# Kernel tuning notes

Hardware: AMD Instinct MI355X
Metric: run time of the kernel (lower is better)

## Reference

```python
import jax, jax.numpy as jnp
import numpy as np

ALPHA = 0.2  # leaky relu slope
NEG = -9e15  # mask fill value from the torch code


def gat_layer(x, adj_mask, W, a):
    """One dense GAT attention head.
    Equivalent math to the torch layer, without materializing the
    [N, N, 2F] a_input tensor: a^T [h_i ; h_j] = (h @ a1)_i + (h @ a2)_j.
    x: [N, Fin], adj_mask: [N, N] bool, W: [Fin, Fout], a: [2*Fout, 1].
    """
    h = x @ W                              # [N, Fout]
    Fo = W.shape[1]
    s_src = h @ a[:Fo, 0]                  # [N]
    s_dst = h @ a[Fo:, 0]                  # [N]
    e = jax.nn.leaky_relu(s_src[:, None] + s_dst[None, :], ALPHA)  # [N, N]
    e = jnp.where(adj_mask, e, NEG)
    attn = jax.nn.softmax(e, axis=1)       # dropout is a no-op in eval mode
    return attn @ h                        # [N, Fout]


def setup_inputs() -> dict:
    key = jax.random.key(0)
    ks = jax.random.split(key, 6)
    N, nfeat, nhid, nclass, nheads = 4096, 512, 64, 32, 8
    x = jax.random.normal(ks[0], (N, nfeat), dtype=jnp.float32)
    adj = jax.random.randint(ks[1], (N, N), 0, 2, dtype=jnp.int32)
    # params scaled like torch uniform(-1/sqrt(fan_in), 1/sqrt(fan_in))
    W_att = jax.random.normal(ks[2], (nheads, nfeat, nhid), dtype=jnp.float32) / np.sqrt(nfeat)
    a_att = jax.random.normal(ks[3], (nheads, 2 * nhid, 1), dtype=jnp.float32) / np.sqrt(2 * nhid)
    W_out = jax.random.normal(ks[4], (nhid * nheads, nclass), dtype=jnp.float32) / np.sqrt(nhid * nheads)
    a_out = jax.random.normal(ks[5], (2 * nclass, 1), dtype=jnp.float32) / np.sqrt(2 * nclass)
    return {"x": x, "adj": adj, "W_att": W_att, "a_att": a_att,
            "W_out": W_out, "a_out": a_out}


def reference(x, adj, W_att, a_att, W_out, a_out):
    adj_mask = adj > 0  # [N, N]
    # multi-head layer, concat=True => elu per head, concat along features
    heads = jax.vmap(lambda W, a: jax.nn.elu(gat_layer(x, adj_mask, W, a)))(W_att, a_att)  # [H, N, nhid]
    H, N, Fh = heads.shape
    hcat = jnp.transpose(heads, (1, 0, 2)).reshape(N, H * Fh)  # [N, H*nhid]
    # output layer, concat=False, then elu applied by GAT.forward
    out = jax.nn.elu(gat_layer(hcat, adj_mask, W_out, a_out))  # [N, nclass]
    return out
```

## Files before the change

### kernel.cpp

```cpp
#include <hip/hip_runtime.h>
#include <math.h>

#define NN 4096
#define CC 512
#define MB (1024*1024)
#define LOG2E 1.4426950408889634f

typedef __attribute__((ext_vector_type(8))) __bf16 bf16x8;
typedef __attribute__((ext_vector_type(4))) float f32x4;
typedef unsigned short ushort_t;
typedef unsigned int uint_t;
typedef unsigned char uchar_t;

#if __has_builtin(__builtin_amdgcn_exp2f)
#define EXP2(x) __builtin_amdgcn_exp2f(x)
#else
#define EXP2(x) exp2f(x)
#endif

static __device__ __forceinline__ float elu1(float x){ return x > 0.f ? x : (__expf(x)-1.f); }
static __device__ __forceinline__ ushort_t f2bf(float f){
    union { float f; uint_t u; } v; v.f = f;
    uint_t r = (v.u + 0x7FFFu + ((v.u >> 16) & 1u)) >> 16;
    return (ushort_t)r;
}
static __device__ __forceinline__ float bf2f(ushort_t h){
    union { uint_t u; float f; } q; q.u = ((uint_t)h) << 16; return q.f;
}

__global__ void k_prepW(const float* __restrict__ Watt,
                        ushort_t* __restrict__ Wh, ushort_t* __restrict__ Wl){
    int idx = blockIdx.x*256 + threadIdx.x;
    int c = idx >> 7, kq = idx & 127, k = kq*4;
    ushort4 h4, l4;
    float v[4];
    #pragma unroll
    for(int j=0;j<4;j++)
        v[j] = Watt[(c>>6)*(512*64) + (k+j)*64 + (c&63)];
    h4.x = f2bf(v[0]); h4.y = f2bf(v[1]); h4.z = f2bf(v[2]); h4.w = f2bf(v[3]);
    l4.x = f2bf(v[0]-bf2f(h4.x)); l4.y = f2bf(v[1]-bf2f(h4.y));
    l4.z = f2bf(v[2]-bf2f(h4.z)); l4.w = f2bf(v[3]-bf2f(h4.w));
    *(ushort4*)&Wh[(size_t)c*512 + k] = h4;
    *(ushort4*)&Wl[(size_t)c*512 + k] = l4;
}

__global__ void k_splitx(const float* __restrict__ x,
                         ushort_t* __restrict__ xh, ushort_t* __restrict__ xl){
    int idx = blockIdx.x*256 + threadIdx.x;
    float4 v = *(const float4*)&x[(size_t)idx*4];
    ushort4 h4, l4;
    h4.x = f2bf(v.x); h4.y = f2bf(v.y); h4.z = f2bf(v.z); h4.w = f2bf(v.w);
    l4.x = f2bf(v.x-bf2f(h4.x)); l4.y = f2bf(v.y-bf2f(h4.y));
    l4.z = f2bf(v.z-bf2f(h4.z)); l4.w = f2bf(v.w-bf2f(h4.w));
    *(ushort4*)&xh[(size_t)idx*4] = h4;
    *(ushort4*)&xl[(size_t)idx*4] = l4;
}

__global__ void k_pack(const int* __restrict__ adj, uint_t* __restrict__ abits){
    int idx = blockIdx.x*256 + threadIdx.x;
    int i = idx >> 7, q = idx & 127;
    const int4* p = (const int4*)&adj[(size_t)i*NN + q*32];
    uint_t m = 0;
    #pragma unroll
    for(int g=0; g<8; g++){
        int4 v = p[g];
        m |= (uint_t)(v.x > 0) << (g*4 + 0);
        m |= (uint_t)(v.y > 0) << (g*4 + 1);
        m |= (uint_t)(v.z > 0) << (g*4 + 2);
        m |= (uint_t)(v.w > 0) << (g*4 + 3);
    }
    abits[idx] = m;
}

__global__ __launch_bounds__(256) void k_gemm1(
        const ushort_t* __restrict__ xh, const ushort_t* __restrict__ xl,
        const ushort_t* __restrict__ Wh, const ushort_t* __restrict__ Wl,
        float* __restrict__ h_all, ushort_t* __restrict__ hT){
    const int t = threadIdx.x;
    const int l = t & 63, wv = t >> 6;
    const int lr = l & 15, lg = l >> 4;
    const int ib = blockIdx.x*64 + wv*16;
    const int j0 = blockIdx.y*64;

    f32x4 acc[4] = {};
    #pragma unroll 2
    for(int ks=0; ks<16; ks++){
        const int kb = ks*32 + lg*8;
        bf16x8 ah = *(const bf16x8*)&xh[(size_t)(ib+lr)*512 + kb];
        bf16x8 al = *(const bf16x8*)&xl[(size_t)(ib+lr)*512 + kb];
        bf16x8 bh[4], bl[4];
        #pragma unroll
        for(int nt=0;nt<4;nt++){
            bh[nt] = *(const bf16x8*)&Wh[(size_t)(j0+nt*16+lr)*512 + kb];
            bl[nt] = *(const bf16x8*)&Wl[(size_t)(j0+nt*16+lr)*512 + kb];
        }
        #pragma unroll
        for(int nt=0;nt<4;nt++){
            acc[nt] = __builtin_amdgcn_mfma_f32_16x16x32_bf16(ah, bh[nt], acc[nt], 0,0,0);
            acc[nt] = __builtin_amdgcn_mfma_f32_16x16x32_bf16(al, bh[nt], acc[nt], 0,0,0);
            acc[nt] = __builtin_amdgcn_mfma_f32_16x16x32_bf16(ah, bl[nt], acc[nt], 0,0,0);
        }
    }
    #pragma unroll
    for(int nt=0;nt<4;nt++){
        const int col = j0 + nt*16 + lr;
        #pragma unroll
        for(int r=0;r<4;r++)
            h_all[(size_t)(ib + lg*4 + r)*512 + col] = acc[nt][r];
        ushort4 o;
        o.x = f2bf(acc[nt][0]); o.y = f2bf(acc[nt][1]);
        o.z = f2bf(acc[nt][2]); o.w = f2bf(acc[nt][3]);
        *(ushort4*)&hT[(size_t)col*NN + ib + lg*4] = o;
    }
}

__global__ void k_scores1(const float* __restrict__ hall, const float* __restrict__ aatt,
                          float* __restrict__ ssrc2, float* __restrict__ sdst2){
    int t = threadIdx.x;
    int hd = t & 7, il = t >> 3;
    int i = blockIdx.x*32 + il;
    const float4* h4 = (const float4*)&hall[(size_t)i*CC + hd*64];
    const float4* a1 = (const float4*)&aatt[hd*128];
    const float4* a2 = (const float4*)&aatt[hd*128 + 64];
    float ss = 0.f, sd = 0.f;
    #pragma unroll
    for(int q=0;q<16;q++){
        float4 h = h4[q], u = a1[q], v = a2[q];
        ss += h.x*u.x + h.y*u.y + h.z*u.z + h.w*u.w;
        sd += h.x*v.x + h.y*v.y + h.z*v.z + h.w*v.w;
    }
    ssrc2[hd*NN + i] = ss*LOG2E;
    sdst2[hd*NN + i] = sd*LOG2E;
}

__global__ __launch_bounds__(256) void k_attn1(
        const ushort_t* __restrict__ hT,
        const float* __restrict__ ssrc2, const float* __restrict__ sdst2,
        const uchar_t* __restrict__ abits,
        float* __restrict__ pnumT, float* __restrict__ pden){
    const int t = threadIdx.x;
    const int l = t & 63, wv = t >> 6;
    const int hd0 = blockIdx.z*2;
    const int i0 = blockIdx.x*32;
    const int jcc = blockIdx.y;
    const int lr = l & 15, lg = l >> 4;

    f32x4 acc[2][2][4] = {};
    f32x4 dacc[2][2] = {};

    float ss[2][2];
    #pragma unroll
    for(int hd=0;hd<2;hd++)
        #pragma unroll
        for(int mh=0;mh<2;mh++)
            ss[hd][mh] = ssrc2[(hd0+hd)*NN + i0 + mh*16 + lr];

    bf16x8 ones;
    #pragma unroll
    for(int e=0;e<8;e++) ones[e] = (__bf16)1.0f;

    const int jwb = jcc*2048 + wv*512;
    const uchar_t* arow0 = &abits[(size_t)(i0 + lr)*512 + jcc*256 + wv*64];
    const uchar_t* arow1 = &abits[(size_t)(i0 + 16 + lr)*512 + jcc*256 + wv*64];

    bf16x8 bA[2][4], bB[2][4];
    float4 sdaA[2], sdbA[2], sdaB[2], sdbB[2];
    uint_t bitsA0, bitsA1, bitsB0, bitsB1;

#define LOAD1(SFX, JT) { \
    const int jb_ = jwb + (JT)*32 + lg*8; \
    _Pragma("unroll") \
    for(int hd=0;hd<2;hd++){ \
        _Pragma("unroll") \
        for(int nt=0;nt<4;nt++) \
            b##SFX[hd][nt] = *(const bf16x8*)&hT[(size_t)((hd0+hd)*64 + nt*16 + lr)*NN + jb_]; \
        sda##SFX[hd] = *(const float4*)&sdst2[(hd0+hd)*NN + jb_]; \
        sdb##SFX[hd] = *(const float4*)&sdst2[(hd0+hd)*NN + jb_ + 4]; \
    } \
    bits##SFX##0 = arow0[(JT)*4 + lg]; \
    bits##SFX##1 = arow1[(JT)*4 + lg]; }

#define COMP1(SFX) { \
    _Pragma("unroll") \
    for(int hd=0;hd<2;hd++){ \
        float sdv[8] = {sda##SFX[hd].x, sda##SFX[hd].y, sda##SFX[hd].z, sda##SFX[hd].w, \
                        sdb##SFX[hd].x, sdb##SFX[hd].y, sdb##SFX[hd].z, sdb##SFX[hd].w}; \
        _Pragma("unroll") \
        for(int mh=0;mh<2;mh++){ \
            const uint_t bits = mh ? bits##SFX##1 : bits##SFX##0; \
            bf16x8 a; \
            _Pragma("unroll") \
            for(int e=0;e<8;e++){ \
                float s_ = ss[hd][mh] + sdv[e]; \
                float t_ = fmaxf(s_, 0.2f*s_); \
                float w_ = EXP2(t_) * (float)((bits >> e) & 1u); \
                a[e] = (__bf16)w_; \
            } \
            _Pragma("unroll") \
            for(int nt=0;nt<4;nt++) \
                acc[hd][mh][nt] = __builtin_amdgcn_mfma_f32_16x16x32_bf16( \
                    a, b##SFX[hd][nt], acc[hd][mh][nt], 0, 0, 0); \
            dacc[hd][mh] = __builtin_amdgcn_mfma_f32_16x16x32_bf16( \
                    a, ones, dacc[hd][mh], 0, 0, 0); \
        } \
    } }

    LOAD1(A, 0);
    for(int jt=0; jt<16; jt+=2){
        LOAD1(B, jt+1);
        COMP1(A);
        if (jt + 2 < 16) LOAD1(A, jt+2);
        COMP1(B);
    }
#undef LOAD1
#undef COMP1

    __shared__ f32x4 red[2][20][64];
    __syncthreads();
    if (wv >= 2){
        #pragma unroll
        for(int hd=0;hd<2;hd++)
            #pragma unroll
            for(int mh=0;mh<2;mh++){
                #pragma unroll
                for(int nt=0;nt<4;nt++) red[wv-2][(hd*2+mh)*4+nt][l] = acc[hd][mh][nt];
                red[wv-2][16 + hd*2+mh][l] = dacc[hd][mh];
            }
    }
    __syncthreads();
    if (wv < 2){
        #pragma unroll
        for(int hd=0;hd<2;hd++)
            #pragma unroll
            for(int mh=0;mh<2;mh++){
                #pragma unroll
                for(int nt=0;nt<4;nt++) acc[hd][mh][nt] += red[wv][(hd*2+mh)*4+nt][l];
                dacc[hd][mh] += red[wv][16 + hd*2+mh][l];
            }
    }
    __syncthreads();
    if (wv == 1){
        #pragma unroll
        for(int hd=0;hd<2;hd++)
            #pragma unroll
            for(int mh=0;mh<2;mh++){
                #pragma unroll
                for(int nt=0;nt<4;nt++) red[0][(hd*2+mh)*4+nt][l] = acc[hd][mh][nt];
                red[0][16 + hd*2+mh][l] = dacc[hd][mh];
            }
    }
    __syncthreads();
    if (wv == 0){
        #pragma unroll
        for(int hd=0;hd<2;hd++)
            #pragma unroll
            for(int mh=0;mh<2;mh++){
                #pragma unroll
                for(int nt=0;nt<4;nt++){
                    f32x4 v = acc[hd][mh][nt] + red[0][(hd*2+mh)*4+nt][l];
                    int col = (hd0+hd)*64 + nt*16 + lr;
                    float4 o = {v[0], v[1], v[2], v[3]};
                    *(float4*)&pnumT[((size_t)jcc*512 + col)*NN + i0 + mh*16 + lg*4] = o;
                }
                f32x4 d = dacc[hd][mh] + red[0][16 + hd*2+mh][l];
                if (lr == 0){
                    #pragma unroll
                    for(int r=0;r<4;r++)
                        pden[((size_t)jcc*8 + hd0+hd)*NN + i0 + mh*16 + lg*4 + r] = d[r];
                }
            }
    }
}

__global__ void k_reduce1T(const float* __restrict__ pnumT, const float* __restrict__ pden,
                           float* __restrict__ hcatT){
    int idx = blockIdx.x*256 + threadIdx.x;
    int c = idx >> 12, i = idx & 4095, hd = c >> 6;
    float s = 0.f, d = 0.f;
    #pragma unroll
    for(int jc=0;jc<2;jc++){
        s += pnumT[((size_t)jc*512 + c)*NN + i];
        d += pden[((size_t)jc*8 + hd)*NN + i];
    }
    hcatT[(size_t)c*NN + i] = elu1(s/d);
}

__global__ __launch_bounds__(256) void k_gemm2(const float* __restrict__ AT,
                                               const float* __restrict__ B,
                                               const float* __restrict__ aout,
                                               ushort_t* __restrict__ h2T,
                                               float* __restrict__ ss2,
                                               float* __restrict__ sd2){
    __shared__ float As[32][32];
    __shared__ float Bs[32][32];
    const int t = threadIdx.x;
    const int i0 = blockIdx.x*32;
    const int ty = t >> 4, tx = t & 15;
    float acc[2][2] = {{0.f,0.f},{0.f,0.f}};
    for(int k0=0;k0<512;k0+=32){
        __syncthreads();
        { int k = t >> 3, i4 = (t & 7)*4;
          *(float4*)&As[k][i4] = *(const float4*)&AT[(size_t)(k0+k)*NN + i0 + i4]; }
        { int k = t >> 3, n4 = (t & 7)*4;
          *(float4*)&Bs[k][n4] = *(const float4*)&B[(size_t)(k0+k)*32 + n4]; }
        __syncthreads();
        #pragma unroll
        for(int k=0;k<32;k++){
            float2 a2 = *(const float2*)&As[k][ty*2];
            float2 b2 = *(const float2*)&Bs[k][tx*2];
            acc[0][0] += a2.x*b2.x; acc[0][1] += a2.x*b2.y;
            acc[1][0] += a2.y*b2.x; acc[1][1] += a2.y*b2.y;
        }
    }
    #pragma unroll
    for(int a=0;a<2;a++){
        #pragma unroll
        for(int b=0;b<2;b++)
            h2T[(size_t)(tx*2+b)*NN + i0 + ty*2 + a] = f2bf(acc[a][b]);
    }
    float a1x = aout[tx*2], a1y = aout[tx*2+1];
    float a2x = aout[32+tx*2], a2y = aout[32+tx*2+1];
    #pragma unroll
    for(int a=0;a<2;a++){
        float ps = acc[a][0]*a1x + acc[a][1]*a1y;
        float pd = acc[a][0]*a2x + acc[a][1]*a2y;
        #pragma unroll
        for(int m=1;m<16;m<<=1){
            ps += __shfl_xor(ps, m);
            pd += __shfl_xor(pd, m);
        }
        if (tx == 0){
            ss2[i0 + ty*2 + a] = ps*LOG2E;
            sd2[i0 + ty*2 + a] = pd*LOG2E;
        }
    }
}

__global__ __launch_bounds__(256) void k_attn2(
        const ushort_t* __restrict__ h2T,
        const float* __restrict__ ss2, const float* __restrict__ sd2,
        const uchar_t* __restrict__ abits,
        float* __restrict__ pnum2T, float* __restrict__ pden2){
    const int t = threadIdx.x;
    const int l = t & 63;
    const int wv = t >> 6;
    const int i0 = blockIdx.x*16;
    const int jc = blockIdx.y;
    const int lr = l & 15, lg = l >> 4;
    const int jcw = jc*4 + wv;

    f32x4 acc[2] = {};
    f32x4 dacc = {};
    const float ss = ss2[i0 + lr];
    bf16x8 ones;
    #pragma unroll
    for(int e=0;e<8;e++) ones[e] = (__bf16)1.0f;

    const uchar_t* arow = &abits[(size_t)(i0+lr)*512 + jc*128 + wv*4];

    bf16x8 bA[2], bB[2];
    float4 sdaA, sdbA, sdaB, sdbB;
    uint_t bitsA, bitsB;

#define LOAD2(SFX, JT) { \
    const int jb_ = jc*1024 + (JT)*128 + wv*32 + lg*8; \
    _Pragma("unroll") \
    for(int nt=0;nt<2;nt++) \
        b##SFX[nt] = *(const bf16x8*)&h2T[(size_t)(nt*16 + lr)*NN + jb_]; \
    sda##SFX = *(const float4*)&sd2[jb_]; \
    sdb##SFX = *(const float4*)&sd2[jb_ + 4]; \
    bits##SFX = arow[(JT)*16 + lg]; }

#define COMP2(SFX) { \
    float sdv[8] = {sda##SFX.x, sda##SFX.y, sda##SFX.z, sda##SFX.w, \
                    sdb##SFX.x, sdb##SFX.y, sdb##SFX.z, sdb##SFX.w}; \
    bf16x8 a; \
    _Pragma("unroll") \
    for(int e=0;e<8;e++){ \
        float s_ = ss + sdv[e]; \
        float t_ = fmaxf(s_, 0.2f*s_); \
        float w_ = EXP2(t_) * (float)((bits##SFX >> e) & 1u); \
        a[e] = (__bf16)w_; \
    } \
    _Pragma("unroll") \
    for(int nt=0;nt<2;nt++) \
        acc[nt] = __builtin_amdgcn_mfma_f32_16x16x32_bf16(a, b##SFX[nt], acc[nt], 0, 0, 0); \
    dacc = __builtin_amdgcn_mfma_f32_16x16x32_bf16(a, ones, dacc, 0, 0, 0); }

    LOAD2(A, 0);
    for(int jt=0; jt<8; jt+=2){
        LOAD2(B, jt+1);
        COMP2(A);
        if (jt + 2 < 8) LOAD2(A, jt+2);
        COMP2(B);
    }
#undef LOAD2
#undef COMP2

    #pragma unroll
    for(int nt=0;nt<2;nt++){
        int col = nt*16 + lr;
        float4 v = {acc[nt][0], acc[nt][1], acc[nt][2], acc[nt][3]};
        *(float4*)&pnum2T[((size_t)jcw*32 + col)*NN + i0 + lg*4] = v;
    }
    if (lr == 0){
        #pragma unroll
        for(int r=0;r<4;r++)
            pden2[(size_t)jcw*NN + i0 + lg*4 + r] = dacc[r];
    }
}

__global__ void k_reduce2(const float* __restrict__ pnum2T, const float* __restrict__ pden2,
                          float* __restrict__ out){
    int idx = blockIdx.x*256 + threadIdx.x;
    int c = idx >> 12, i = idx & 4095;
    float s = 0.f, d = 0.f;
    #pragma unroll
    for(int jcw=0;jcw<16;jcw++){
        s += pnum2T[((size_t)jcw*32 + c)*NN + i];
        d += pden2[(size_t)jcw*NN + i];
    }
    out[(size_t)i*32 + c] = elu1(s/d);
}

extern "C" void kernel_launch(void* const* d_in, const int* in_sizes, int n_in,
                              void* d_out, int out_size, void* d_ws, size_t ws_size,
                              hipStream_t stream){
    const float* x    = (const float*)d_in[0];
    const int*   adj  = (const int*)  d_in[1];
    const float* Watt = (const float*)d_in[2];
    const float* aatt = (const float*)d_in[3];
    const float* Wout = (const float*)d_in[4];
    const float* aout = (const float*)d_in[5];
    float* out = (float*)d_out;
    char* ws = (char*)d_ws;

    float*    h_all = (float*)   (ws + (size_t) 0*MB);
    float*    hcatT = (float*)   (ws + (size_t) 0*MB);
    ushort_t* Whi   = (ushort_t*)(ws + (size_t) 8*MB);
    ushort_t* Wlo   = (ushort_t*)(ws + (size_t) 8*MB + 512*1024);
    float*    ssrc2 = (float*)   (ws + (size_t) 9*MB);
    float*    sdst2 = (float*)   (ws + (size_t)10*MB);
    ushort_t* hT    = (ushort_t*)(ws + (size_t)11*MB);
    uint_t*   abits = (uint_t*)  (ws + (size_t)15*MB);
    float*    ss2   = (float*)   (ws + (size_t)18*MB);
    float*    sd2   = (float*)   (ws + (size_t)19*MB);
    ushort_t* h2T   = (ushort_t*)(ws + (size_t)20*MB);
    float*    pden  = (float*)   (ws + (size_t)21*MB);
    float*    pden2 = (float*)   (ws + (size_t)21*MB + 512*1024);
    float*    pnumT = (float*)   (ws + (size_t)22*MB);
    float*    pnum2T= pnumT;
    ushort_t* xh    = (ushort_t*)(ws + (size_t)38*MB);
    ushort_t* xl    = (ushort_t*)(ws + (size_t)42*MB);
    if (ws_size < (size_t)55*MB) return;

    k_prepW   <<<256, 256, 0, stream>>>(Watt, Whi, Wlo);
    k_splitx  <<<2048, 256, 0, stream>>>(x, xh, xl);
    k_pack    <<<2048, 256, 0, stream>>>(adj, abits);
    k_gemm1   <<<dim3(64,8), 256, 0, stream>>>(xh, xl, Whi, Wlo, h_all, hT);
    k_scores1 <<<128, 256, 0, stream>>>(h_all, aatt, ssrc2, sdst2);
    k_attn1   <<<dim3(128,2,4), 256, 0, stream>>>(hT, ssrc2, sdst2, (const uchar_t*)abits, pnumT, pden);
    k_reduce1T<<<8192, 256, 0, stream>>>(pnumT, pden, hcatT);
    k_gemm2   <<<128, 256, 0, stream>>>(hcatT, Wout, aout, h2T, ss2, sd2);
    k_attn2   <<<dim3(256,4), 256, 0, stream>>>(h2T, ss2, sd2, (const uchar_t*)abits, pnum2T, pden2);
    k_reduce2 <<<512, 256, 0, stream>>>(pnum2T, pden2, out);
}
```

Baseline: 299.4 us.

## Fuse score computation into GEMM1 and retile both attention kernels

Computes the source/destination attention scores in the GEMM1 epilogue with a lane-shuffle reduction, which removes the fp32 h_all write and the separate k_scores1 kernel. k_attn1 now processes one head per block with 64 rows instead of two heads with 32 rows. The j-dimension split changes from 2 to 4 chunks, so each loaded hT tile is reused across more rows. k_attn2 is retiled the same way, with 64 rows per block and a shared-memory cross-wave reduction, which halves the partial sums that k_reduce2 has to read. The cost is more accumulator registers per thread, which may lower occupancy, and more partial-sum traffic in the first reduce.

Result: faster. 263.0 us (-12.2%).

```diff
diff --git a/kernel.cpp b/kernel.cpp
--- a/kernel.cpp
+++ b/kernel.cpp
@@ -75,12 +75,15 @@
 __global__ __launch_bounds__(256) void k_gemm1(
         const ushort_t* __restrict__ xh, const ushort_t* __restrict__ xl,
         const ushort_t* __restrict__ Wh, const ushort_t* __restrict__ Wl,
-        float* __restrict__ h_all, ushort_t* __restrict__ hT){
+        const float* __restrict__ aatt,
+        ushort_t* __restrict__ hT,
+        float* __restrict__ ssrc2, float* __restrict__ sdst2){
     const int t = threadIdx.x;
     const int l = t & 63, wv = t >> 6;
     const int lr = l & 15, lg = l >> 4;
     const int ib = blockIdx.x*64 + wv*16;
-    const int j0 = blockIdx.y*64;
+    const int hd = blockIdx.y;
+    const int j0 = hd*64;
 
     f32x4 acc[4] = {};
     #pragma unroll 2
@@ -104,33 +107,31 @@
     #pragma unroll
     for(int nt=0;nt<4;nt++){
         const int col = j0 + nt*16 + lr;
-        #pragma unroll
-        for(int r=0;r<4;r++)
-            h_all[(size_t)(ib + lg*4 + r)*512 + col] = acc[nt][r];
         ushort4 o;
         o.x = f2bf(acc[nt][0]); o.y = f2bf(acc[nt][1]);
         o.z = f2bf(acc[nt][2]); o.w = f2bf(acc[nt][3]);
         *(ushort4*)&hT[(size_t)col*NN + ib + lg*4] = o;
     }
-}
-
-__global__ void k_scores1(const float* __restrict__ hall, const float* __restrict__ aatt,
-                          float* __restrict__ ssrc2, float* __restrict__ sdst2){
-    int t = threadIdx.x;
-    int hd = t & 7, il = t >> 3;
-    int i = blockIdx.x*32 + il;
-    const float4* h4 = (const float4*)&hall[(size_t)i*CC + hd*64];
-    const float4* a1 = (const float4*)&aatt[hd*128];
-    const float4* a2 = (const float4*)&aatt[hd*128 + 64];
-    float ss = 0.f, sd = 0.f;
-    #pragma unroll
-    for(int q=0;q<16;q++){
-        float4 h = h4[q], u = a1[q], v = a2[q];
-        ss += h.x*u.x + h.y*u.y + h.z*u.z + h.w*u.w;
-        sd += h.x*v.x + h.y*v.y + h.z*v.z + h.w*v.w;
-    }
-    ssrc2[hd*NN + i] = ss*LOG2E;
-    sdst2[hd*NN + i] = sd*LOG2E;
+    float a1v[4], a2v[4];
+    #pragma unroll
+    for(int nt=0;nt<4;nt++){
+        a1v[nt] = aatt[hd*128 + nt*16 + lr];
+        a2v[nt] = aatt[hd*128 + 64 + nt*16 + lr];
+    }
+    #pragma unroll
+    for(int r=0;r<4;r++){
+        float ps = acc[0][r]*a1v[0] + acc[1][r]*a1v[1] + acc[2][r]*a1v[2] + acc[3][r]*a1v[3];
+        float pd = acc[0][r]*a2v[0] + acc[1][r]*a2v[1] + acc[2][r]*a2v[2] + acc[3][r]*a2v[3];
+        #pragma unroll
+        for(int m=1;m<16;m<<=1){
+            ps += __shfl_xor(ps, m);
+            pd += __shfl_xor(pd, m);
+        }
+        if (lr == 0){
+            ssrc2[hd*NN + ib + lg*4 + r] = ps*LOG2E;
+            sdst2[hd*NN + ib + lg*4 + r] = pd*LOG2E;
+        }
+    }
 }
 
 __global__ __launch_bounds__(256) void k_attn1(
@@ -140,76 +141,71 @@
         float* __restrict__ pnumT, float* __restrict__ pden){
     const int t = threadIdx.x;
     const int l = t & 63, wv = t >> 6;
-    const int hd0 = blockIdx.z*2;
-    const int i0 = blockIdx.x*32;
+    const int hd = blockIdx.z;
+    const int i0 = blockIdx.x*64;
     const int jcc = blockIdx.y;
     const int lr = l & 15, lg = l >> 4;
 
-    f32x4 acc[2][2][4] = {};
-    f32x4 dacc[2][2] = {};
-
-    float ss[2][2];
-    #pragma unroll
-    for(int hd=0;hd<2;hd++)
-        #pragma unroll
-        for(int mh=0;mh<2;mh++)
-            ss[hd][mh] = ssrc2[(hd0+hd)*NN + i0 + mh*16 + lr];
+    f32x4 acc[4][4] = {};
+    f32x4 dacc[4] = {};
+
+    float ss[4];
+    #pragma unroll
+    for(int mh=0;mh<4;mh++)
+        ss[mh] = ssrc2[hd*NN + i0 + mh*16 + lr];
 
     bf16x8 ones;
     #pragma unroll
     for(int e=0;e<8;e++) ones[e] = (__bf16)1.0f;
 
-    const int jwb = jcc*2048 + wv*512;
-    const uchar_t* arow0 = &abits[(size_t)(i0 + lr)*512 + jcc*256 + wv*64];
-    const uchar_t* arow1 = &abits[(size_t)(i0 + 16 + lr)*512 + jcc*256 + wv*64];
-
-    bf16x8 bA[2][4], bB[2][4];
-    float4 sdaA[2], sdbA[2], sdaB[2], sdbB[2];
-    uint_t bitsA0, bitsA1, bitsB0, bitsB1;
+    const int jwb = jcc*1024 + wv*256;
+    const uchar_t* arow[4];
+    #pragma unroll
+    for(int mh=0;mh<4;mh++)
+        arow[mh] = &abits[(size_t)(i0 + mh*16 + lr)*512 + (jwb >> 3)];
+
+    bf16x8 bA[4], bB[4];
+    float4 sdaA, sdbA, sdaB, sdbB;
+    uint_t bitsA[4], bitsB[4];
 
 #define LOAD1(SFX, JT) { \
     const int jb_ = jwb + (JT)*32 + lg*8; \
     _Pragma("unroll") \
-    for(int hd=0;hd<2;hd++){ \
+    for(int nt=0;nt<4;nt++) \
+        b##SFX[nt] = *(const bf16x8*)&hT[(size_t)(hd*64 + nt*16 + lr)*NN + jb_]; \
+    sda##SFX = *(const float4*)&sdst2[hd*NN + jb_]; \
+    sdb##SFX = *(const float4*)&sdst2[hd*NN + jb_ + 4]; \
+    _Pragma("unroll") \
+    for(int mh=0;mh<4;mh++) \
+        bits##SFX[mh] = arow[mh][(JT)*4 + lg]; }
+
+#define COMP1(SFX) { \
+    float sdv[8] = {sda##SFX.x, sda##SFX.y, sda##SFX.z, sda##SFX.w, \
+                    sdb##SFX.x, sdb##SFX.y, sdb##SFX.z, sdb##SFX.w}; \
+    _Pragma("unroll") \
+    for(int mh=0;mh<4;mh++){ \
+        const uint_t bits = bits##SFX[mh]; \
+        bf16x8 a; \
+        _Pragma("unroll") \
+        for(int e=0;e<8;e++){ \
+            float s_ = ss[mh] + sdv[e]; \
+            float t_ = fmaxf(s_, 0.2f*s_); \
+            float w_ = EXP2(t_) * (float)((bits >> e) & 1u); \
+            a[e] = (__bf16)w_; \
+        } \
         _Pragma("unroll") \
         for(int nt=0;nt<4;nt++) \
-            b##SFX[hd][nt] = *(const bf16x8*)&hT[(size_t)((hd0+hd)*64 + nt*16 + lr)*NN + jb_]; \
-        sda##SFX[hd] = *(const float4*)&sdst2[(hd0+hd)*NN + jb_]; \
-        sdb##SFX[hd] = *(const float4*)&sdst2[(hd0+hd)*NN + jb_ + 4]; \
-    } \
-    bits##SFX##0 = arow0[(JT)*4 + lg]; \
-    bits##SFX##1 = arow1[(JT)*4 + lg]; }
-
-#define COMP1(SFX) { \
-    _Pragma("unroll") \
-    for(int hd=0;hd<2;hd++){ \
-        float sdv[8] = {sda##SFX[hd].x, sda##SFX[hd].y, sda##SFX[hd].z, sda##SFX[hd].w, \
-                        sdb##SFX[hd].x, sdb##SFX[hd].y, sdb##SFX[hd].z, sdb##SFX[hd].w}; \
-        _Pragma("unroll") \
-        for(int mh=0;mh<2;mh++){ \
-            const uint_t bits = mh ? bits##SFX##1 : bits##SFX##0; \
-            bf16x8 a; \
-            _Pragma("unroll") \
-            for(int e=0;e<8;e++){ \
-                float s_ = ss[hd][mh] + sdv[e]; \
-                float t_ = fmaxf(s_, 0.2f*s_); \
-                float w_ = EXP2(t_) * (float)((bits >> e) & 1u); \
-                a[e] = (__bf16)w_; \
-            } \
-            _Pragma("unroll") \
-            for(int nt=0;nt<4;nt++) \
-                acc[hd][mh][nt] = __builtin_amdgcn_mfma_f32_16x16x32_bf16( \
-                    a, b##SFX[hd][nt], acc[hd][mh][nt], 0, 0, 0); \
-            dacc[hd][mh] = __builtin_amdgcn_mfma_f32_16x16x32_bf16( \
-                    a, ones, dacc[hd][mh], 0, 0, 0); \
-        } \
+            acc[mh][nt] = __builtin_amdgcn_mfma_f32_16x16x32_bf16( \
+                a, b##SFX[nt], acc[mh][nt], 0, 0, 0); \
+        dacc[mh] = __builtin_amdgcn_mfma_f32_16x16x32_bf16( \
+                a, ones, dacc[mh], 0, 0, 0); \
     } }
 
     LOAD1(A, 0);
-    for(int jt=0; jt<16; jt+=2){
+    for(int jt=0; jt<8; jt+=2){
         LOAD1(B, jt+1);
         COMP1(A);
-        if (jt + 2 < 16) LOAD1(A, jt+2);
+        if (jt + 2 < 8) LOAD1(A, jt+2);
         COMP1(B);
     }
 #undef LOAD1
@@ -219,56 +215,48 @@
     __syncthreads();
     if (wv >= 2){
         #pragma unroll
-        for(int hd=0;hd<2;hd++)
-            #pragma unroll
-            for(int mh=0;mh<2;mh++){
+        for(int mh=0;mh<4;mh++){
+            #pragma unroll
+            for(int nt=0;nt<4;nt++) red[wv-2][mh*4+nt][l] = acc[mh][nt];
+            red[wv-2][16+mh][l] = dacc[mh];
+        }
+    }
+    __syncthreads();
+    if (wv < 2){
+        #pragma unroll
+        for(int mh=0;mh<4;mh++){
+            #pragma unroll
+            for(int nt=0;nt<4;nt++) acc[mh][nt] += red[wv][mh*4+nt][l];
+            dacc[mh] += red[wv][16+mh][l];
+        }
+    }
+    __syncthreads();
+    if (wv == 1){
+        #pragma unroll
+        for(int mh=0;mh<4;mh++){
+            #pragma unroll
+            for(int nt=0;nt<4;nt++) red[0][mh*4+nt][l] = acc[mh][nt];
+            red[0][16+mh][l] = dacc[mh];
+        }
+    }
+    __syncthreads();
+    if (wv == 0){
+        #pragma unroll
+        for(int mh=0;mh<4;mh++){
+            #pragma unroll
+            for(int nt=0;nt<4;nt++){
+                f32x4 v = acc[mh][nt] + red[0][mh*4+nt][l];
+                int col = hd*64 + nt*16 + lr;
+                float4 o = {v[0], v[1], v[2], v[3]};
+                *(float4*)&pnumT[((size_t)jcc*512 + col)*NN + i0 + mh*16 + lg*4] = o;
+            }
+            f32x4 d = dacc[mh] + red[0][16+mh][l];
+            if (lr == 0){
                 #pragma unroll
-                for(int nt=0;nt<4;nt++) red[wv-2][(hd*2+mh)*4+nt][l] = acc[hd][mh][nt];
-                red[wv-2][16 + hd*2+mh][l] = dacc[hd][mh];
+                for(int r=0;r<4;r++)
+                    pden[((size_t)jcc*8 + hd)*NN + i0 + mh*16 + lg*4 + r] = d[r];
             }
-    }
-    __syncthreads();
-    if (wv < 2){
-        #pragma unroll
-        for(int hd=0;hd<2;hd++)
-            #pragma unroll
-            for(int mh=0;mh<2;mh++){
-                #pragma unroll
-                for(int nt=0;nt<4;nt++) acc[hd][mh][nt] += red[wv][(hd*2+mh)*4+nt][l];
-                dacc[hd][mh] += red[wv][16 + hd*2+mh][l];
-            }
-    }
-    __syncthreads();
-    if (wv == 1){
-        #pragma unroll
-        for(int hd=0;hd<2;hd++)
-            #pragma unroll
-            for(int mh=0;mh<2;mh++){
-                #pragma unroll
-                for(int nt=0;nt<4;nt++) red[0][(hd*2+mh)*4+nt][l] = acc[hd][mh][nt];
-                red[0][16 + hd*2+mh][l] = dacc[hd][mh];
-            }
-    }
-    __syncthreads();
-    if (wv == 0){
-        #pragma unroll
-        for(int hd=0;hd<2;hd++)
-            #pragma unroll
-            for(int mh=0;mh<2;mh++){
-                #pragma unroll
-                for(int nt=0;nt<4;nt++){
-                    f32x4 v = acc[hd][mh][nt] + red[0][(hd*2+mh)*4+nt][l];
-                    int col = (hd0+hd)*64 + nt*16 + lr;
-                    float4 o = {v[0], v[1], v[2], v[3]};
-                    *(float4*)&pnumT[((size_t)jcc*512 + col)*NN + i0 + mh*16 + lg*4] = o;
-                }
-                f32x4 d = dacc[hd][mh] + red[0][16 + hd*2+mh][l];
-                if (lr == 0){
-                    #pragma unroll
-                    for(int r=0;r<4;r++)
-                        pden[((size_t)jcc*8 + hd0+hd)*NN + i0 + mh*16 + lg*4 + r] = d[r];
-                }
-            }
+        }
     }
 }
 
@@ -278,7 +266,7 @@
     int c = idx >> 12, i = idx & 4095, hd = c >> 6;
     float s = 0.f, d = 0.f;
     #pragma unroll
-    for(int jc=0;jc<2;jc++){
+    for(int jc=0;jc<4;jc++){
         s += pnumT[((size_t)jc*512 + c)*NN + i];
         d += pden[((size_t)jc*8 + hd)*NN + i];
     }
@@ -342,71 +330,122 @@
         const uchar_t* __restrict__ abits,
         float* __restrict__ pnum2T, float* __restrict__ pden2){
     const int t = threadIdx.x;
-    const int l = t & 63;
-    const int wv = t >> 6;
-    const int i0 = blockIdx.x*16;
+    const int l = t & 63, wv = t >> 6;
+    const int i0 = blockIdx.x*64;
     const int jc = blockIdx.y;
     const int lr = l & 15, lg = l >> 4;
-    const int jcw = jc*4 + wv;
-
-    f32x4 acc[2] = {};
-    f32x4 dacc = {};
-    const float ss = ss2[i0 + lr];
+
+    f32x4 acc[4][2] = {};
+    f32x4 dacc[4] = {};
+
+    float ss[4];
+    #pragma unroll
+    for(int mh=0;mh<4;mh++)
+        ss[mh] = ss2[i0 + mh*16 + lr];
+
     bf16x8 ones;
     #pragma unroll
     for(int e=0;e<8;e++) ones[e] = (__bf16)1.0f;
 
-    const uchar_t* arow = &abits[(size_t)(i0+lr)*512 + jc*128 + wv*4];
+    const int jwb = jc*512 + wv*128;
+    const uchar_t* arow[4];
+    #pragma unroll
+    for(int mh=0;mh<4;mh++)
+        arow[mh] = &abits[(size_t)(i0 + mh*16 + lr)*512 + (jwb >> 3)];
 
     bf16x8 bA[2], bB[2];
     float4 sdaA, sdbA, sdaB, sdbB;
-    uint_t bitsA, bitsB;
+    uint_t bitsA[4], bitsB[4];
 
 #define LOAD2(SFX, JT) { \
-    const int jb_ = jc*1024 + (JT)*128 + wv*32 + lg*8; \
+    const int jb_ = jwb + (JT)*32 + lg*8; \
     _Pragma("unroll") \
     for(int nt=0;nt<2;nt++) \
         b##SFX[nt] = *(const bf16x8*)&h2T[(size_t)(nt*16 + lr)*NN + jb_]; \
     sda##SFX = *(const float4*)&sd2[jb_]; \
     sdb##SFX = *(const float4*)&sd2[jb_ + 4]; \
-    bits##SFX = arow[(JT)*16 + lg]; }
+    _Pragma("unroll") \
+    for(int mh=0;mh<4;mh++) \
+        bits##SFX[mh] = arow[mh][(JT)*4 + lg]; }
 
 #define COMP2(SFX) { \
     float sdv[8] = {sda##SFX.x, sda##SFX.y, sda##SFX.z, sda##SFX.w, \
                     sdb##SFX.x, sdb##SFX.y, sdb##SFX.z, sdb##SFX.w}; \
-    bf16x8 a; \
     _Pragma("unroll") \
-    for(int e=0;e<8;e++){ \
-        float s_ = ss + sdv[e]; \
-        float t_ = fmaxf(s_, 0.2f*s_); \
-        float w_ = EXP2(t_) * (float)((bits##SFX >> e) & 1u); \
-        a[e] = (__bf16)w_; \
-    } \
-    _Pragma("unroll") \
-    for(int nt=0;nt<2;nt++) \
-        acc[nt] = __builtin_amdgcn_mfma_f32_16x16x32_bf16(a, b##SFX[nt], acc[nt], 0, 0, 0); \
-    dacc = __builtin_amdgcn_mfma_f32_16x16x32_bf16(a, ones, dacc, 0, 0, 0); }
+    for(int mh=0;mh<4;mh++){ \
+        const uint_t bits = bits##SFX[mh]; \
+        bf16x8 a; \
+        _Pragma("unroll") \
+        for(int e=0;e<8;e++){ \
+            float s_ = ss[mh] + sdv[e]; \
+            float t_ = fmaxf(s_, 0.2f*s_); \
+            float w_ = EXP2(t_) * (float)((bits >> e) & 1u); \
+            a[e] = (__bf16)w_; \
+        } \
+        _Pragma("unroll") \
+        for(int nt=0;nt<2;nt++) \
+            acc[mh][nt] = __builtin_amdgcn_mfma_f32_16x16x32_bf16( \
+                a, b##SFX[nt], acc[mh][nt], 0, 0, 0); \
+        dacc[mh] = __builtin_amdgcn_mfma_f32_16x16x32_bf16( \
+                a, ones, dacc[mh], 0, 0, 0); \
+    } }
 
     LOAD2(A, 0);
-    for(int jt=0; jt<8; jt+=2){
+    for(int jt=0; jt<4; jt+=2){
         LOAD2(B, jt+1);
         COMP2(A);
-        if (jt + 2 < 8) LOAD2(A, jt+2);
+        if (jt + 2 < 4) LOAD2(A, jt+2);
         COMP2(B);
     }
 #undef LOAD2
 #undef COMP2
 
-    #pragma unroll
-    for(int nt=0;nt<2;nt++){
-        int col = nt*16 + lr;
-        float4 v = {acc[nt][0], acc[nt][1], acc[nt][2], acc[nt][3]};
-        *(float4*)&pnum2T[((size_t)jcw*32 + col)*NN + i0 + lg*4] = v;
-    }
-    if (lr == 0){
-        #pragma unroll
-        for(int r=0;r<4;r++)
-            pden2[(size_t)jcw*NN + i0 + lg*4 + r] = dacc[r];
+    __shared__ f32x4 red2[2][12][64];
+    __syncthreads();
+    if (wv >= 2){
+        #pragma unroll
+        for(int mh=0;mh<4;mh++){
+            #pragma unroll
+            for(int nt=0;nt<2;nt++) red2[wv-2][mh*2+nt][l] = acc[mh][nt];
+            red2[wv-2][8+mh][l] = dacc[mh];
+        }
+    }
+    __syncthreads();
+    if (wv < 2){
+        #pragma unroll
+        for(int mh=0;mh<4;mh++){
+            #pragma unroll
+            for(int nt=0;nt<2;nt++) acc[mh][nt] += red2[wv][mh*2+nt][l];
+            dacc[mh] += red2[wv][8+mh][l];
+        }
+    }
+    __syncthreads();
+    if (wv == 1){
+        #pragma unroll
+        for(int mh=0;mh<4;mh++){
+            #pragma unroll
+            for(int nt=0;nt<2;nt++) red2[0][mh*2+nt][l] = acc[mh][nt];
+            red2[0][8+mh][l] = dacc[mh];
+        }
+    }
+    __syncthreads();
+    if (wv == 0){
+        #pragma unroll
+        for(int mh=0;mh<4;mh++){
+            #pragma unroll
+            for(int nt=0;nt<2;nt++){
+                f32x4 v = acc[mh][nt] + red2[0][mh*2+nt][l];
+                int col = nt*16 + lr;
+                float4 o = {v[0], v[1], v[2], v[3]};
+                *(float4*)&pnum2T[((size_t)jc*32 + col)*NN + i0 + mh*16 + lg*4] = o;
+            }
+            f32x4 d = dacc[mh] + red2[0][8+mh][l];
+            if (lr == 0){
+                #pragma unroll
+                for(int r=0;r<4;r++)
+                    pden2[(size_t)jc*NN + i0 + mh*16 + lg*4 + r] = d[r];
+            }
+        }
     }
 }
 
@@ -416,9 +455,9 @@
     int c = idx >> 12, i = idx & 4095;
     float s = 0.f, d = 0.f;
     #pragma unroll
-    for(int jcw=0;jcw<16;jcw++){
-        s += pnum2T[((size_t)jcw*32 + c)*NN + i];
-        d += pden2[(size_t)jcw*NN + i];
+    for(int jc=0;jc<8;jc++){
+        s += pnum2T[((size_t)jc*32 + c)*NN + i];
+        d += pden2[(size_t)jc*NN + i];
     }
     out[(size_t)i*32 + c] = elu1(s/d);
 }
@@ -435,7 +474,6 @@
     float* out = (float*)d_out;
     char* ws = (char*)d_ws;
 
-    float*    h_all = (float*)   (ws + (size_t) 0*MB);
     float*    hcatT = (float*)   (ws + (size_t) 0*MB);
     ushort_t* Whi   = (ushort_t*)(ws + (size_t) 8*MB);
     ushort_t* Wlo   = (ushort_t*)(ws + (size_t) 8*MB + 512*1024);
@@ -450,18 +488,17 @@
     float*    pden2 = (float*)   (ws + (size_t)21*MB + 512*1024);
     float*    pnumT = (float*)   (ws + (size_t)22*MB);
     float*    pnum2T= pnumT;
-    ushort_t* xh    = (ushort_t*)(ws + (size_t)38*MB);
-    ushort_t* xl    = (ushort_t*)(ws + (size_t)42*MB);
+    ushort_t* xh    = (ushort_t*)(ws + (size_t)46*MB);
+    ushort_t* xl    = (ushort_t*)(ws + (size_t)50*MB);
     if (ws_size < (size_t)55*MB) return;
 
     k_prepW   <<<256, 256, 0, stream>>>(Watt, Whi, Wlo);
     k_splitx  <<<2048, 256, 0, stream>>>(x, xh, xl);
     k_pack    <<<2048, 256, 0, stream>>>(adj, abits);
-    k_gemm1   <<<dim3(64,8), 256, 0, stream>>>(xh, xl, Whi, Wlo, h_all, hT);
-    k_scores1 <<<128, 256, 0, stream>>>(h_all, aatt, ssrc2, sdst2);
-    k_attn1   <<<dim3(128,2,4), 256, 0, stream>>>(hT, ssrc2, sdst2, (const uchar_t*)abits, pnumT, pden);
+    k_gemm1   <<<dim3(64,8), 256, 0, stream>>>(xh, xl, Whi, Wlo, aatt, hT, ssrc2, sdst2);
+    k_attn1   <<<dim3(64,4,8), 256, 0, stream>>>(hT, ssrc2, sdst2, (const uchar_t*)abits, pnumT, pden);
     k_reduce1T<<<8192, 256, 0, stream>>>(pnumT, pden, hcatT);
     k_gemm2   <<<128, 256, 0, stream>>>(hcatT, Wout, aout, h2T, ss2, sd2);
-    k_attn2   <<<dim3(256,4), 256, 0, stream>>>(h2T, ss2, sd2, (const uchar_t*)abits, pnum2T, pden2);
+    k_attn2   <<<dim3(64,8), 256, 0, stream>>>(h2T, ss2, sd2, (const uchar_t*)abits, pnum2T, pden2);
     k_reduce2 <<<512, 256, 0, stream>>>(pnum2T, pden2, out);
 }
```
